# Performance work log

Hardware: AMD Instinct MI355X
Metric: run time of the kernel (lower is better)

Reference implementation:

```python
import jax, jax.numpy as jnp
import numpy as np

N_NODES = 50000
N_EDGES = 300000
HIDDEN = 256
Z_DIM = 128
N_LAYERS = 3
NUM_GRAPHS = 16
EPS = 1e-5


def setup_inputs() -> dict:
    key = jax.random.key(0)
    ks = jax.random.split(key, 16)
    s = 0.05
    inp = {
        "voxel_pos": jax.random.normal(ks[0], (N_NODES, 3), jnp.float32),
        "edge_index": jax.random.randint(ks[1], (2, N_EDGES), 0, N_NODES),
        "batch_index": jnp.sort(jax.random.randint(ks[2], (N_NODES,), 0, NUM_GRAPHS)),
        # input projection Linear(3, H) + GroupNorm(1, H) affine
        "W_in": jax.random.normal(ks[3], (3, HIDDEN), jnp.float32) * s,
        "b_in": jnp.zeros((HIDDEN,), jnp.float32),
        "g_in": jnp.ones((HIDDEN,), jnp.float32),
        "be_in": jnp.zeros((HIDDEN,), jnp.float32),
        # stacked GCNConv weights/biases and per-layer GroupNorm affines
        "conv_W": jax.random.normal(ks[4], (N_LAYERS, HIDDEN, HIDDEN), jnp.float32) * s,
        "conv_b": jnp.zeros((N_LAYERS, HIDDEN), jnp.float32),
        "gn_g": jnp.ones((N_LAYERS, HIDDEN), jnp.float32),
        "gn_b": jnp.zeros((N_LAYERS, HIDDEN), jnp.float32),
        # output MLP: Linear(H,H) -> ReLU -> GroupNorm -> Linear(H, Z)
        "W_o1": jax.random.normal(ks[5], (HIDDEN, HIDDEN), jnp.float32) * s,
        "b_o1": jnp.zeros((HIDDEN,), jnp.float32),
        "g_o": jnp.ones((HIDDEN,), jnp.float32),
        "be_o": jnp.zeros((HIDDEN,), jnp.float32),
        "W_o2": jax.random.normal(ks[6], (HIDDEN, Z_DIM), jnp.float32) * s,
        "b_o2": jnp.zeros((Z_DIM,), jnp.float32),
    }
    return inp


def group_norm(x, g, b):
    # GroupNorm(1, C) on (N, C): normalize over channels per node (biased var)
    mu = jnp.mean(x, axis=-1, keepdims=True)
    var = jnp.mean(jnp.square(x - mu), axis=-1, keepdims=True)
    return (x - mu) * jax.lax.rsqrt(var + EPS) * g + b


def reference(voxel_pos, edge_index, batch_index, W_in, b_in, g_in, be_in,
              conv_W, conv_b, gn_g, gn_b, W_o1, b_o1, g_o, be_o, W_o2, b_o2):
    n = voxel_pos.shape[0]
    loop = jnp.arange(n, dtype=edge_index.dtype)
    src = jnp.concatenate([edge_index[0], loop])  # A + I self-loops (PyG GCNConv default)
    dst = jnp.concatenate([edge_index[1], loop])
    deg = jax.ops.segment_sum(jnp.ones_like(dst, jnp.float32), dst, num_segments=n)
    dinv = jnp.where(deg > 0, jax.lax.rsqrt(jnp.maximum(deg, 1.0)), 0.0)
    enorm = dinv[src] * dinv[dst]  # D^{-1/2} (A+I) D^{-1/2} edge weights

    # input_proj: Linear -> ReLU -> GroupNorm
    x = group_norm(jax.nn.relu(voxel_pos @ W_in + b_in), g_in, be_in)

    for l in range(N_LAYERS):
        identity = x
        h = x @ conv_W[l]                      # GCNConv linear transform
        msg = h[src] * enorm[:, None]          # gather + scale (E+N, H)
        h = jax.ops.segment_sum(msg, dst, num_segments=n) + conv_b[l]
        x = jax.nn.relu(group_norm(h, gn_g[l], gn_b[l])) + identity

    # global mean pool per graph
    summed = jax.ops.segment_sum(x, batch_index, num_segments=NUM_GRAPHS)
    counts = jax.ops.segment_sum(jnp.ones((n,), jnp.float32), batch_index, num_segments=NUM_GRAPHS)
    pooled = summed / jnp.maximum(counts, 1.0)[:, None]

    h = group_norm(jax.nn.relu(pooled @ W_o1 + b_o1), g_o, be_o)
    return h @ W_o2 + b_o2
```

## Files before the change

### kernel.cpp

```cpp
#include <hip/hip_runtime.h>
#include <hip/hip_bf16.h>

#define N_NODES 50000
#define N_EDGES 300000
#define HIDDEN 256
#define ZDIM 128
#define NLAYERS 3
#define NGRAPHS 16
#define EPS 1e-5f
#define NSCANBLK 196

#define OFF_POS    0
#define OFF_WIN    150000
#define OFF_BIN    150768
#define OFF_GIN    151024
#define OFF_BEIN   151280
#define OFF_CONVB  348144
#define OFF_GNG    348912
#define OFF_GNB    349680
#define OFF_WO1    350448
#define OFF_BO1    415984
#define OFF_GO     416240
#define OFF_BEO    416496
#define OFF_WO2    416752
#define OFF_BO2    449520
#define PARAMS_TOTAL 449648

typedef __attribute__((ext_vector_type(8))) short short8;
typedef __attribute__((ext_vector_type(4))) float floatx4;

__device__ inline float wave_reduce_sum(float v){
#pragma unroll
  for (int off = 32; off; off >>= 1) v += __shfl_xor(v, off);
  return v;
}

__device__ inline ushort f2bf(float f){
  __hip_bfloat16 t = __float2bfloat16(f);
  return *(ushort*)&t;
}
__device__ inline float bflo(unsigned int u){ return __uint_as_float(u << 16); }
__device__ inline float bfhi(unsigned int u){ return __uint_as_float(u & 0xffff0000u); }

__device__ inline void gload_lds16(const void* g, void* l){
  __builtin_amdgcn_global_load_lds((const __attribute__((address_space(1))) void*)g,
                                   (__attribute__((address_space(3))) void*)l, 16, 0, 0);
}

struct PrepArgs { const void* src[14]; int n[14]; int off[14]; const void* win; const void* convw; };

__global__ __launch_bounds__(256) void k_prep(PrepArgs a, float* __restrict__ params,
                                              ushort* __restrict__ Wt, int* __restrict__ flag){
  __shared__ int sf;
  int tid = threadIdx.x;
  if (tid == 0) sf = 0;
  __syncthreads();
  const unsigned short* w = (const unsigned short*)a.win;
  for (int i = tid; i < 768; i += 256){
    int e = (w[i] >> 7) & 0xff;
    if (e >= 148) atomicOr(&sf, 1);
  }
  __syncthreads();
  const bool isf32 = (sf != 0);
  if (blockIdx.x == 0 && tid == 0) *flag = sf;

  int stride = gridDim.x * blockDim.x;
  int t0 = blockIdx.x * blockDim.x + tid;
  for (int s = 0; s < 14; ++s){
    const void* src = a.src[s];
    int n = a.n[s];
    float* dst = params + a.off[s];
    if (isf32){
      const float* f = (const float*)src;
      for (int i = t0; i < n; i += stride) dst[i] = f[i];
    } else {
      const unsigned short* u = (const unsigned short*)src;
      for (int i = t0; i < n; i += stride) dst[i] = bflo(u[i]);
    }
  }
  for (int idx = t0; idx < NLAYERS * 65536; idx += stride){
    int l = idx >> 16, rem = idx & 65535, n = rem >> 8, k = rem & 255;
    int si = l * 65536 + k * 256 + n;
    float v = isf32 ? ((const float*)a.convw)[si] : bflo(((const unsigned short*)a.convw)[si]);
    Wt[idx] = f2bf(v);
  }
}

__global__ void k_init(int* __restrict__ deg, int* __restrict__ fill,
                       float* __restrict__ pooled, float* __restrict__ counts){
  int i = blockIdx.x * blockDim.x + threadIdx.x;
  if (i < N_NODES){ deg[i] = 1; fill[i] = 0; }
  if (i < NGRAPHS * 256) pooled[i] = 0.f;
  if (i < NGRAPHS) counts[i] = 0.f;
}

__global__ void k_deg(const int* __restrict__ dst, int* __restrict__ deg){
  int e = blockIdx.x * blockDim.x + threadIdx.x;
  if (e < N_EDGES) atomicAdd(&deg[dst[e]], 1);
}

__global__ __launch_bounds__(256) void k_scan1(const int* __restrict__ deg, int* __restrict__ row_start,
                                               int* __restrict__ bsum, float* __restrict__ dinv){
  __shared__ int sd[256];
  int tid = threadIdx.x;
  int i = blockIdx.x * 256 + tid;
  int v = (i < N_NODES) ? deg[i] : 0;
  if (i < N_NODES) dinv[i] = rsqrtf((float)v);
  sd[tid] = v;
  __syncthreads();
#pragma unroll
  for (int off = 1; off < 256; off <<= 1){
    int t = (tid >= off) ? sd[tid - off] : 0;
    __syncthreads();
    sd[tid] += t;
    __syncthreads();
  }
  if (i < N_NODES) row_start[i] = sd[tid];
  if (tid == 255) bsum[blockIdx.x] = sd[255];
}

__global__ __launch_bounds__(256) void k_scan2(const int* __restrict__ bsum, int* __restrict__ boff,
                                               int* __restrict__ row_start){
  __shared__ int sd[256];
  int tid = threadIdx.x;
  int v = (tid < NSCANBLK) ? bsum[tid] : 0;
  sd[tid] = v;
  __syncthreads();
#pragma unroll
  for (int off = 1; off < 256; off <<= 1){
    int t = (tid >= off) ? sd[tid - off] : 0;
    __syncthreads();
    sd[tid] += t;
    __syncthreads();
  }
  if (tid < NSCANBLK) boff[tid] = sd[tid] - v;
  if (tid == NSCANBLK - 1) row_start[N_NODES] = sd[tid];
}

__global__ __launch_bounds__(256) void k_scan3(const int* __restrict__ deg, const int* __restrict__ boff,
                                               int* __restrict__ row_start){
  int i = blockIdx.x * 256 + threadIdx.x;
  if (i < N_NODES) row_start[i] = row_start[i] + boff[blockIdx.x] - deg[i];
}

__global__ void k_fill(const int* __restrict__ src, const int* __restrict__ dst,
                       const int* __restrict__ row_start, int* __restrict__ fill,
                       const float* __restrict__ dinv,
                       int* __restrict__ csr_src, float* __restrict__ csr_w){
  int t = blockIdx.x * blockDim.x + threadIdx.x;
  if (t >= N_EDGES + N_NODES) return;
  int s, d;
  if (t < N_EDGES){ s = src[t]; d = dst[t]; }
  else            { s = t - N_EDGES; d = s; }
  int pos = row_start[d] + atomicAdd(&fill[d], 1);
  csr_src[pos] = s;
  csr_w[pos] = dinv[s] * dinv[d];
}

__global__ __launch_bounds__(256) void k_input_proj(const float* __restrict__ params,
                                                    ushort* __restrict__ x_bf){
  int lane = threadIdx.x & 63;
  int node = (blockIdx.x << 2) + (threadIdx.x >> 6);
  if (node >= N_NODES) return;
  const float* pos = params + OFF_POS + node * 3;
  float px = pos[0], py = pos[1], pz = pos[2];
  int c = lane * 4;
  const float* w0 = params + OFF_WIN;
  float v[4];
#pragma unroll
  for (int j = 0; j < 4; ++j){
    float t = params[OFF_BIN + c + j];
    t = fmaf(px, w0[c + j], t);
    t = fmaf(py, w0[256 + c + j], t);
    t = fmaf(pz, w0[512 + c + j], t);
    v[j] = fmaxf(t, 0.f);
  }
  float s  = v[0] + v[1] + v[2] + v[3];
  float ss = v[0]*v[0] + v[1]*v[1] + v[2]*v[2] + v[3]*v[3];
  s = wave_reduce_sum(s); ss = wave_reduce_sum(ss);
  float mean = s * (1.f/256.f);
  float var  = ss * (1.f/256.f) - mean * mean;
  float inv  = rsqrtf(var + EPS);
  float4 o;
  o.x = (v[0]-mean)*inv*params[OFF_GIN+c+0] + params[OFF_BEIN+c+0];
  o.y = (v[1]-mean)*inv*params[OFF_GIN+c+1] + params[OFF_BEIN+c+1];
  o.z = (v[2]-mean)*inv*params[OFF_GIN+c+2] + params[OFF_BEIN+c+2];
  o.w = (v[3]-mean)*inv*params[OFF_GIN+c+3] + params[OFF_BEIN+c+3];
  ushort4 ob = { f2bf(o.x), f2bf(o.y), f2bf(o.z), f2bf(o.w) };
  *(ushort4*)(x_bf + node * 256 + c) = ob;
}

#define GBM 128
__global__ __launch_bounds__(256) void k_gemm_bf(const ushort* __restrict__ A, const ushort* __restrict__ Bt,
                                                 ushort* __restrict__ Cb, int M){
  __shared__ __align__(16) ushort Sh[2 * GBM * 64];
  ushort* As = Sh;
  ushort* Bs = Sh + GBM * 64;
  int tid = threadIdx.x;
  int wave = tid >> 6, lane = tid & 63;
  int wr = wave >> 1, wc = wave & 1;
  int row0 = blockIdx.y * GBM;
  int col0 = blockIdx.x * GBM;
  int q = lane >> 4, l15 = lane & 15;
  int srow = lane >> 3;
  int sg   = lane & 7;
  floatx4 acc[4][4] = {};
  for (int k0 = 0; k0 < 256; k0 += 64){
    __syncthreads();
#pragma unroll
    for (int t = 0; t < 4; ++t){
      int rg = wave * 4 + t;
      int r  = rg * 8 + srow;
      int gs = sg ^ (r & 7);
      const ushort* ga = A  + (size_t)(row0 + r) * 256 + k0 + gs * 8;
      const ushort* gb = Bt + (size_t)(col0 + r) * 256 + k0 + gs * 8;
      gload_lds16(ga, As + rg * 512);
      gload_lds16(gb, Bs + rg * 512);
    }
    __syncthreads();
#pragma unroll
    for (int kk = 0; kk < 64; kk += 32){
      short8 af[4], bfr[4];
#pragma unroll
      for (int i = 0; i < 4; ++i){
        int R = wr * 64 + i * 16 + l15;
        int bg = (kk >> 3) + q;
        af[i] = *(const short8*)(As + R * 64 + ((bg ^ (R & 7)) << 3));
      }
#pragma unroll
      for (int j = 0; j < 4; ++j){
        int C = wc * 64 + j * 16 + l15;
        int bg = (kk >> 3) + q;
        bfr[j] = *(const short8*)(Bs + C * 64 + ((bg ^ (C & 7)) << 3));
      }
#pragma unroll
      for (int i = 0; i < 4; ++i)
#pragma unroll
        for (int j = 0; j < 4; ++j)
          acc[i][j] = __builtin_amdgcn_mfma_f32_16x16x32_bf16(af[i], bfr[j], acc[i][j], 0, 0, 0);
    }
  }
#pragma unroll
  for (int i = 0; i < 4; ++i){
#pragma unroll
    for (int r = 0; r < 4; ++r){
      int row = row0 + wr * 64 + i * 16 + q * 4 + r;
      if (row < M){
#pragma unroll
        for (int j = 0; j < 4; ++j){
          int col = col0 + wc * 64 + j * 16 + l15;
          Cb[row * 256 + col] = f2bf(acc[i][j][r]);
        }
      }
    }
  }
}

__global__ __launch_bounds__(256) void k_agg_norm(const ushort* __restrict__ hb, ushort* __restrict__ x_bf,
    const int* __restrict__ row_start, const int* __restrict__ csr_src, const float* __restrict__ csr_w,
    const float* __restrict__ params, int layer){
  int lane = threadIdx.x & 63;
  int node = (blockIdx.x << 2) + (threadIdx.x >> 6);
  if (node >= N_NODES) return;
  int c = lane * 4;
  float a0 = 0.f, a1 = 0.f, a2 = 0.f, a3 = 0.f;
  int p0 = row_start[node], p1 = row_start[node + 1];
  int p = p0;
  for (; p + 4 <= p1; p += 4){
    int s0 = csr_src[p],     s1 = csr_src[p + 1];
    int s2 = csr_src[p + 2], s3 = csr_src[p + 3];
    float w0 = csr_w[p],     w1 = csr_w[p + 1];
    float w2 = csr_w[p + 2], w3 = csr_w[p + 3];
    uint2 v0 = *(const uint2*)(hb + (size_t)s0 * 256 + c);
    uint2 v1 = *(const uint2*)(hb + (size_t)s1 * 256 + c);
    uint2 v2 = *(const uint2*)(hb + (size_t)s2 * 256 + c);
    uint2 v3 = *(const uint2*)(hb + (size_t)s3 * 256 + c);
    a0 = fmaf(w0, bflo(v0.x), a0); a1 = fmaf(w0, bfhi(v0.x), a1);
    a2 = fmaf(w0, bflo(v0.y), a2); a3 = fmaf(w0, bfhi(v0.y), a3);
    a0 = fmaf(w1, bflo(v1.x), a0); a1 = fmaf(w1, bfhi(v1.x), a1);
    a2 = fmaf(w1, bflo(v1.y), a2); a3 = fmaf(w1, bfhi(v1.y), a3);
    a0 = fmaf(w2, bflo(v2.x), a0); a1 = fmaf(w2, bfhi(v2.x), a1);
    a2 = fmaf(w2, bflo(v2.y), a2); a3 = fmaf(w2, bfhi(v2.y), a3);
    a0 = fmaf(w3, bflo(v3.x), a0); a1 = fmaf(w3, bfhi(v3.x), a1);
    a2 = fmaf(w3, bflo(v3.y), a2); a3 = fmaf(w3, bfhi(v3.y), a3);
  }
  for (; p < p1; ++p){
    int s0 = csr_src[p];
    float w0 = csr_w[p];
    uint2 v0 = *(const uint2*)(hb + (size_t)s0 * 256 + c);
    a0 = fmaf(w0, bflo(v0.x), a0); a1 = fmaf(w0, bfhi(v0.x), a1);
    a2 = fmaf(w0, bflo(v0.y), a2); a3 = fmaf(w0, bfhi(v0.y), a3);
  }
  const float* cb = params + OFF_CONVB + layer * 256;
  float v[4] = { a0 + cb[c], a1 + cb[c+1], a2 + cb[c+2], a3 + cb[c+3] };
  float s  = v[0] + v[1] + v[2] + v[3];
  float ss = v[0]*v[0] + v[1]*v[1] + v[2]*v[2] + v[3]*v[3];
  s = wave_reduce_sum(s); ss = wave_reduce_sum(ss);
  float mean = s * (1.f/256.f);
  float var  = ss * (1.f/256.f) - mean * mean;
  float inv  = rsqrtf(var + EPS);
  const float* g = params + OFF_GNG + layer * 256;
  const float* b = params + OFF_GNB + layer * 256;
  uint2 xo = *(uint2*)(x_bf + (size_t)node * 256 + c);
  float o0 = fmaxf((v[0]-mean)*inv*g[c+0] + b[c+0], 0.f) + bflo(xo.x);
  float o1 = fmaxf((v[1]-mean)*inv*g[c+1] + b[c+1], 0.f) + bfhi(xo.x);
  float o2 = fmaxf((v[2]-mean)*inv*g[c+2] + b[c+2], 0.f) + bflo(xo.y);
  float o3 = fmaxf((v[3]-mean)*inv*g[c+3] + b[c+3], 0.f) + bfhi(xo.y);
  ushort4 ob = { f2bf(o0), f2bf(o1), f2bf(o2), f2bf(o3) };
  *(ushort4*)(x_bf + (size_t)node * 256 + c) = ob;
}

#define PBLK 256
__global__ __launch_bounds__(256) void k_pool(const ushort* __restrict__ x_bf, const int* __restrict__ batch,
                                              float* __restrict__ pooled, float* __restrict__ counts){
  __shared__ float lacc[NGRAPHS][256];
  __shared__ float lcnt[NGRAPHS];
  int tid = threadIdx.x;
  int wave = tid >> 6, lane = tid & 63;
  int c = lane * 4;
#pragma unroll
  for (int g = 0; g < NGRAPHS; ++g) lacc[g][tid] = 0.f;
  if (tid < NGRAPHS) lcnt[tid] = 0.f;
  __syncthreads();

  int n0 = blockIdx.x * PBLK + wave * 64;
  if (n0 < N_NODES){
    int n1 = min(n0 + 64, N_NODES);
    int b0 = batch[n0], b1 = batch[n1 - 1];
    float a0 = 0.f, a1 = 0.f, a2 = 0.f, a3 = 0.f;
    if (b0 == b1){
      int i = n0;
      for (; i + 8 <= n1; i += 8){
        uint2 v[8];
#pragma unroll
        for (int j = 0; j < 8; ++j) v[j] = *(const uint2*)(x_bf + (size_t)(i + j) * 256 + c);
#pragma unroll
        for (int j = 0; j < 8; ++j){
          a0 += bflo(v[j].x); a1 += bfhi(v[j].x);
          a2 += bflo(v[j].y); a3 += bfhi(v[j].y);
        }
      }
      for (; i < n1; ++i){
        uint2 v = *(const uint2*)(x_bf + (size_t)i * 256 + c);
        a0 += bflo(v.x); a1 += bfhi(v.x); a2 += bflo(v.y); a3 += bfhi(v.y);
      }
      atomicAdd(&lacc[b0][c + 0], a0); atomicAdd(&lacc[b0][c + 1], a1);
      atomicAdd(&lacc[b0][c + 2], a2); atomicAdd(&lacc[b0][c + 3], a3);
      if (lane == 0) atomicAdd(&lcnt[b0], (float)(n1 - n0));
    } else {
      int cur = b0, cnt = 0;
      for (int i = n0; i < n1; ++i){
        int g = batch[i];
        if (g != cur){
          atomicAdd(&lacc[cur][c + 0], a0); atomicAdd(&lacc[cur][c + 1], a1);
          atomicAdd(&lacc[cur][c + 2], a2); atomicAdd(&lacc[cur][c + 3], a3);
          if (lane == 0) atomicAdd(&lcnt[cur], (float)cnt);
          a0 = a1 = a2 = a3 = 0.f; cnt = 0; cur = g;
        }
        uint2 v = *(const uint2*)(x_bf + (size_t)i * 256 + c);
        a0 += bflo(v.x); a1 += bfhi(v.x); a2 += bflo(v.y); a3 += bfhi(v.y);
        cnt++;
      }
      atomicAdd(&lacc[cur][c + 0], a0); atomicAdd(&lacc[cur][c + 1], a1);
      atomicAdd(&lacc[cur][c + 2], a2); atomicAdd(&lacc[cur][c + 3], a3);
      if (lane == 0) atomicAdd(&lcnt[cur], (float)cnt);
    }
  }
  __syncthreads();

  int base = blockIdx.x * PBLK;
  if (base < N_NODES){
    int gmin = batch[base];
    int gmax = batch[min(base + PBLK, N_NODES) - 1];
    for (int g = gmin; g <= gmax; ++g){
      float v = lacc[g][tid];
      if (v != 0.f) atomicAdd(&pooled[g * 256 + tid], v);
      if (tid == 0 && lcnt[g] > 0.f) atomicAdd(&counts[g], lcnt[g]);
    }
  }
}

__global__ __launch_bounds__(256) void k_head(const float* __restrict__ pooled, const float* __restrict__ counts,
    const float* __restrict__ params, void* __restrict__ out, const int* __restrict__ flag){
  __shared__ float m[256];
  __shared__ float hh[256];
  __shared__ float red[2][4];
  int g = blockIdx.x, tid = threadIdx.x;
  float cnt = fmaxf(counts[g], 1.f);
  m[tid] = pooled[g * 256 + tid] / cnt;
  __syncthreads();
  const float* W1 = params + OFF_WO1;
  float acc = params[OFF_BO1 + tid];
  for (int k = 0; k < 256; ++k) acc = fmaf(m[k], W1[k * 256 + tid], acc);
  acc = fmaxf(acc, 0.f);
  float s = wave_reduce_sum(acc), ss = wave_reduce_sum(acc * acc);
  int wv = tid >> 6, lane = tid & 63;
  if (lane == 0){ red[0][wv] = s; red[1][wv] = ss; }
  __syncthreads();
  float S  = red[0][0] + red[0][1] + red[0][2] + red[0][3];
  float SS = red[1][0] + red[1][1] + red[1][2] + red[1][3];
  float mean = S * (1.f/256.f);
  float var  = SS * (1.f/256.f) - mean * mean;
  float inv  = rsqrtf(var + EPS);
  float hn = (acc - mean) * inv * params[OFF_GO + tid] + params[OFF_BEO + tid];
  hh[tid] = hn;
  __syncthreads();
  if (tid < ZDIM){
    const float* W2 = params + OFF_WO2;
    float o = params[OFF_BO2 + tid];
    for (int k = 0; k < 256; ++k) o = fmaf(hh[k], W2[k * 128 + tid], o);
    if (*flag) ((float*)out)[g * 128 + tid] = o;
    else       ((__hip_bfloat16*)out)[g * 128 + tid] = __float2bfloat16(o);
  }
}

extern "C" void kernel_launch(void* const* d_in, const int* in_sizes, int n_in,
                              void* d_out, int out_size, void* d_ws, size_t ws_size,
                              hipStream_t stream){
  size_t o = 0;
  auto alloc = [&](size_t bytes)->size_t{ size_t r = o; o = (o + bytes + 255) & ~(size_t)255; return r; };
  size_t off_flag   = alloc(4);
  size_t off_deg    = alloc((size_t)N_NODES * 4);
  size_t off_dinv   = alloc((size_t)N_NODES * 4);
  size_t off_rs     = alloc((size_t)(N_NODES + 1) * 4);
  size_t off_fill   = alloc((size_t)N_NODES * 4);
  size_t off_bsum   = alloc((size_t)NSCANBLK * 4);
  size_t off_boff   = alloc((size_t)NSCANBLK * 4);
  size_t off_csrs   = alloc((size_t)(N_EDGES + N_NODES) * 4);
  size_t off_csrw   = alloc((size_t)(N_EDGES + N_NODES) * 4);
  size_t off_params = alloc((size_t)PARAMS_TOTAL * 4);
  size_t off_xbf    = alloc((size_t)N_NODES * HIDDEN * 2);
  size_t off_hbf    = alloc((size_t)N_NODES * HIDDEN * 2);
  size_t off_wt     = alloc((size_t)NLAYERS * HIDDEN * HIDDEN * 2);
  size_t off_pool   = alloc((size_t)NGRAPHS * 256 * 4);
  size_t off_cnt    = alloc((size_t)NGRAPHS * 4);
  if (o > ws_size) return;

  char* ws = (char*)d_ws;
  int*    flag     = (int*)(ws + off_flag);
  int*    deg      = (int*)(ws + off_deg);
  float*  dinv     = (float*)(ws + off_dinv);
  int*    row_start= (int*)(ws + off_rs);
  int*    fill     = (int*)(ws + off_fill);
  int*    bsum     = (int*)(ws + off_bsum);
  int*    boff     = (int*)(ws + off_boff);
  int*    csr_src  = (int*)(ws + off_csrs);
  float*  csr_w    = (float*)(ws + off_csrw);
  float*  params   = (float*)(ws + off_params);
  ushort* x_bf     = (ushort*)(ws + off_xbf);
  ushort* h_bf     = (ushort*)(ws + off_hbf);
  ushort* Wt       = (ushort*)(ws + off_wt);
  float*  pooled   = (float*)(ws + off_pool);
  float*  counts   = (float*)(ws + off_cnt);

  const int* edge_src = (const int*)d_in[1];
  const int* edge_dst = (const int*)d_in[1] + N_EDGES;
  const int* batch    = (const int*)d_in[2];

  PrepArgs pa;
  const int srcIdx[14] = {0,3,4,5,6,8,9,10,11,12,13,14,15,16};
  const int ns[14]     = {150000,768,256,256,256,768,768,768,65536,256,256,256,32768,128};
  const int offs[14]   = {OFF_POS,OFF_WIN,OFF_BIN,OFF_GIN,OFF_BEIN,OFF_CONVB,OFF_GNG,OFF_GNB,
                          OFF_WO1,OFF_BO1,OFF_GO,OFF_BEO,OFF_WO2,OFF_BO2};
  for (int i = 0; i < 14; ++i){ pa.src[i] = d_in[srcIdx[i]]; pa.n[i] = ns[i]; pa.off[i] = offs[i]; }
  pa.win = d_in[3]; pa.convw = d_in[7];
  k_prep<<<512, 256, 0, stream>>>(pa, params, Wt, flag);

  k_init<<<(N_NODES + 255) / 256, 256, 0, stream>>>(deg, fill, pooled, counts);
  k_deg<<<(N_EDGES + 255) / 256, 256, 0, stream>>>(edge_dst, deg);
  k_scan1<<<NSCANBLK, 256, 0, stream>>>(deg, row_start, bsum, dinv);
  k_scan2<<<1, 256, 0, stream>>>(bsum, boff, row_start);
  k_scan3<<<NSCANBLK, 256, 0, stream>>>(deg, boff, row_start);
  k_fill<<<(N_EDGES + N_NODES + 255) / 256, 256, 0, stream>>>(edge_src, edge_dst, row_start, fill,
                                                              dinv, csr_src, csr_w);
  k_input_proj<<<N_NODES / 4, 256, 0, stream>>>(params, x_bf);

  dim3 ggrid(2, (N_NODES + GBM - 1) / GBM);
  for (int l = 0; l < NLAYERS; ++l){
    k_gemm_bf<<<ggrid, 256, 0, stream>>>(x_bf, Wt + l * 65536, h_bf, N_NODES);
    k_agg_norm<<<N_NODES / 4, 256, 0, stream>>>(h_bf, x_bf, row_start, csr_src, csr_w, params, l);
  }

  k_pool<<<(N_NODES + PBLK - 1) / PBLK, 256, 0, stream>>>(x_bf, batch, pooled, counts);
  k_head<<<NGRAPHS, 256, 0, stream>>>(pooled, counts, params, d_out, flag);
}
```

Before: 352.7 us.

## Fuse aggregation, GEMM and GroupNorm into one per-layer kernel via aggregate-first reorder

Each GCN layer now aggregates neighbour features first (A·X), stores the aggregated rows for a 64-node tile in shared memory, multiplies by the layer weight with MFMA, then applies bias, GroupNorm, ReLU and the residual in the epilogue, with ping-pong x buffers. This removes the intermediate h round trip through global memory and one kernel launch per layer. The trade-offs are that the aggregated features are rounded to bf16 before the GEMM, the whole weight matrix is streamed per 64-row block, epilogue stores are scalar 2-byte writes, and the large shared-memory footprint may lower occupancy for the latency-bound gather.

```diff
diff --git a/kernel.cpp b/kernel.cpp
--- a/kernel.cpp
+++ b/kernel.cpp
@@ -190,46 +190,86 @@
   *(ushort4*)(x_bf + node * 256 + c) = ob;
 }
 
-#define GBM 128
-__global__ __launch_bounds__(256) void k_gemm_bf(const ushort* __restrict__ A, const ushort* __restrict__ Bt,
-                                                 ushort* __restrict__ Cb, int M){
-  __shared__ __align__(16) ushort Sh[2 * GBM * 64];
-  ushort* As = Sh;
-  ushort* Bs = Sh + GBM * 64;
+#define LBM 64
+__global__ __launch_bounds__(256) void k_layer(const ushort* __restrict__ xin, ushort* __restrict__ xout,
+    const int* __restrict__ row_start, const int* __restrict__ csr_src, const float* __restrict__ csr_w,
+    const ushort* __restrict__ Bt, const float* __restrict__ params, int layer){
+  __shared__ __align__(16) ushort As[LBM * 256];
+  __shared__ __align__(16) ushort Bs[256 * 64];
+  __shared__ float rsum[4][LBM], rsq[4][LBM];
+  __shared__ float mmean[LBM], minv[LBM];
   int tid = threadIdx.x;
   int wave = tid >> 6, lane = tid & 63;
-  int wr = wave >> 1, wc = wave & 1;
-  int row0 = blockIdx.y * GBM;
-  int col0 = blockIdx.x * GBM;
   int q = lane >> 4, l15 = lane & 15;
-  int srow = lane >> 3;
-  int sg   = lane & 7;
+  int srow = lane >> 3, sg = lane & 7;
+  int row0 = blockIdx.x * LBM;
+
+#pragma unroll
+  for (int t = 0; t < 8; ++t){
+    int rg = wave * 8 + t;
+    int r = rg * 8 + srow;
+    int gs = sg ^ (r & 7);
+    gload_lds16(Bt + (size_t)r * 256 + 0 + gs * 8, Bs + rg * 512);
+  }
+
+  int c = lane * 4;
+  for (int t = 0; t < 16; ++t){
+    int nloc = wave * 16 + t;
+    int node = row0 + nloc;
+    float a0 = 0.f, a1 = 0.f, a2 = 0.f, a3 = 0.f;
+    if (node < N_NODES){
+      int p0 = row_start[node], p1 = row_start[node + 1];
+      int p = p0;
+      for (; p + 8 <= p1; p += 8){
+        int s[8]; float w[8]; uint2 v[8];
+#pragma unroll
+        for (int j = 0; j < 8; ++j){ s[j] = csr_src[p + j]; w[j] = csr_w[p + j]; }
+#pragma unroll
+        for (int j = 0; j < 8; ++j) v[j] = *(const uint2*)(xin + (size_t)s[j] * 256 + c);
+#pragma unroll
+        for (int j = 0; j < 8; ++j){
+          a0 = fmaf(w[j], bflo(v[j].x), a0); a1 = fmaf(w[j], bfhi(v[j].x), a1);
+          a2 = fmaf(w[j], bflo(v[j].y), a2); a3 = fmaf(w[j], bfhi(v[j].y), a3);
+        }
+      }
+      for (; p < p1; ++p){
+        int s0 = csr_src[p]; float w0 = csr_w[p];
+        uint2 v0 = *(const uint2*)(xin + (size_t)s0 * 256 + c);
+        a0 = fmaf(w0, bflo(v0.x), a0); a1 = fmaf(w0, bfhi(v0.x), a1);
+        a2 = fmaf(w0, bflo(v0.y), a2); a3 = fmaf(w0, bfhi(v0.y), a3);
+      }
+    }
+    int gp = (lane >> 1) ^ (nloc & 7);
+    ushort4 mv = { f2bf(a0), f2bf(a1), f2bf(a2), f2bf(a3) };
+    *(ushort4*)(As + nloc * 256 + gp * 8 + (lane & 1) * 4) = mv;
+  }
+  __syncthreads();
+
   floatx4 acc[4][4] = {};
   for (int k0 = 0; k0 < 256; k0 += 64){
-    __syncthreads();
-#pragma unroll
-    for (int t = 0; t < 4; ++t){
-      int rg = wave * 4 + t;
-      int r  = rg * 8 + srow;
-      int gs = sg ^ (r & 7);
-      const ushort* ga = A  + (size_t)(row0 + r) * 256 + k0 + gs * 8;
-      const ushort* gb = Bt + (size_t)(col0 + r) * 256 + k0 + gs * 8;
-      gload_lds16(ga, As + rg * 512);
-      gload_lds16(gb, Bs + rg * 512);
-    }
-    __syncthreads();
+    if (k0 > 0){
+      __syncthreads();
+#pragma unroll
+      for (int t = 0; t < 8; ++t){
+        int rg = wave * 8 + t;
+        int r = rg * 8 + srow;
+        int gs = sg ^ (r & 7);
+        gload_lds16(Bt + (size_t)r * 256 + k0 + gs * 8, Bs + rg * 512);
+      }
+      __syncthreads();
+    }
 #pragma unroll
     for (int kk = 0; kk < 64; kk += 32){
       short8 af[4], bfr[4];
 #pragma unroll
       for (int i = 0; i < 4; ++i){
-        int R = wr * 64 + i * 16 + l15;
-        int bg = (kk >> 3) + q;
-        af[i] = *(const short8*)(As + R * 64 + ((bg ^ (R & 7)) << 3));
+        int R = i * 16 + l15;
+        int lg = ((k0 + kk) >> 3) + q;
+        af[i] = *(const short8*)(As + R * 256 + ((lg ^ (R & 7)) << 3));
       }
 #pragma unroll
       for (int j = 0; j < 4; ++j){
-        int C = wc * 64 + j * 16 + l15;
+        int C = wave * 64 + j * 16 + l15;
         int bg = (kk >> 3) + q;
         bfr[j] = *(const short8*)(Bs + C * 64 + ((bg ^ (C & 7)) << 3));
       }
@@ -240,74 +280,78 @@
           acc[i][j] = __builtin_amdgcn_mfma_f32_16x16x32_bf16(af[i], bfr[j], acc[i][j], 0, 0, 0);
     }
   }
+
+  const float* cb = params + OFF_CONVB + layer * 256;
+  const float* gw = params + OFF_GNG  + layer * 256;
+  const float* bw = params + OFF_GNB  + layer * 256;
+  float cbv[4], gv[4], bv[4];
+#pragma unroll
+  for (int j = 0; j < 4; ++j){
+    int C = wave * 64 + j * 16 + l15;
+    cbv[j] = cb[C]; gv[j] = gw[C]; bv[j] = bw[C];
+  }
+  float psum[4][4], psq[4][4];
+#pragma unroll
+  for (int i = 0; i < 4; ++i)
+#pragma unroll
+    for (int r = 0; r < 4; ++r){
+      float s = 0.f, s2 = 0.f;
+#pragma unroll
+      for (int j = 0; j < 4; ++j){
+        float v = acc[i][j][r] + cbv[j];
+        acc[i][j][r] = v;
+        s += v; s2 += v * v;
+      }
+      psum[i][r] = s; psq[i][r] = s2;
+    }
+#pragma unroll
+  for (int off = 1; off < 16; off <<= 1){
+#pragma unroll
+    for (int i = 0; i < 4; ++i)
+#pragma unroll
+      for (int r = 0; r < 4; ++r){
+        psum[i][r] += __shfl_xor(psum[i][r], off);
+        psq[i][r]  += __shfl_xor(psq[i][r], off);
+      }
+  }
+  if (l15 == 0){
+#pragma unroll
+    for (int i = 0; i < 4; ++i)
+#pragma unroll
+      for (int r = 0; r < 4; ++r){
+        int row = i * 16 + q * 4 + r;
+        rsum[wave][row] = psum[i][r];
+        rsq[wave][row]  = psq[i][r];
+      }
+  }
+  __syncthreads();
+  if (tid < LBM){
+    float t0 = rsum[0][tid] + rsum[1][tid] + rsum[2][tid] + rsum[3][tid];
+    float t1 = rsq[0][tid]  + rsq[1][tid]  + rsq[2][tid]  + rsq[3][tid];
+    float mean = t0 * (1.f/256.f);
+    float var  = t1 * (1.f/256.f) - mean * mean;
+    mmean[tid] = mean;
+    minv[tid]  = rsqrtf(var + EPS);
+  }
+  __syncthreads();
 #pragma unroll
   for (int i = 0; i < 4; ++i){
 #pragma unroll
     for (int r = 0; r < 4; ++r){
-      int row = row0 + wr * 64 + i * 16 + q * 4 + r;
-      if (row < M){
+      int row = i * 16 + q * 4 + r;
+      int grow = row0 + row;
+      if (grow < N_NODES){
+        float mean = mmean[row], inv = minv[row];
 #pragma unroll
         for (int j = 0; j < 4; ++j){
-          int col = col0 + wc * 64 + j * 16 + l15;
-          Cb[row * 256 + col] = f2bf(acc[i][j][r]);
+          int col = wave * 64 + j * 16 + l15;
+          float vn = (acc[i][j][r] - mean) * inv * gv[j] + bv[j];
+          float o = fmaxf(vn, 0.f) + bflo((unsigned int)xin[(size_t)grow * 256 + col]);
+          xout[(size_t)grow * 256 + col] = f2bf(o);
         }
       }
     }
   }
-}
-
-__global__ __launch_bounds__(256) void k_agg_norm(const ushort* __restrict__ hb, ushort* __restrict__ x_bf,
-    const int* __restrict__ row_start, const int* __restrict__ csr_src, const float* __restrict__ csr_w,
-    const float* __restrict__ params, int layer){
-  int lane = threadIdx.x & 63;
-  int node = (blockIdx.x << 2) + (threadIdx.x >> 6);
-  if (node >= N_NODES) return;
-  int c = lane * 4;
-  float a0 = 0.f, a1 = 0.f, a2 = 0.f, a3 = 0.f;
-  int p0 = row_start[node], p1 = row_start[node + 1];
-  int p = p0;
-  for (; p + 4 <= p1; p += 4){
-    int s0 = csr_src[p],     s1 = csr_src[p + 1];
-    int s2 = csr_src[p + 2], s3 = csr_src[p + 3];
-    float w0 = csr_w[p],     w1 = csr_w[p + 1];
-    float w2 = csr_w[p + 2], w3 = csr_w[p + 3];
-    uint2 v0 = *(const uint2*)(hb + (size_t)s0 * 256 + c);
-    uint2 v1 = *(const uint2*)(hb + (size_t)s1 * 256 + c);
-    uint2 v2 = *(const uint2*)(hb + (size_t)s2 * 256 + c);
-    uint2 v3 = *(const uint2*)(hb + (size_t)s3 * 256 + c);
-    a0 = fmaf(w0, bflo(v0.x), a0); a1 = fmaf(w0, bfhi(v0.x), a1);
-    a2 = fmaf(w0, bflo(v0.y), a2); a3 = fmaf(w0, bfhi(v0.y), a3);
-    a0 = fmaf(w1, bflo(v1.x), a0); a1 = fmaf(w1, bfhi(v1.x), a1);
-    a2 = fmaf(w1, bflo(v1.y), a2); a3 = fmaf(w1, bfhi(v1.y), a3);
-    a0 = fmaf(w2, bflo(v2.x), a0); a1 = fmaf(w2, bfhi(v2.x), a1);
-    a2 = fmaf(w2, bflo(v2.y), a2); a3 = fmaf(w2, bfhi(v2.y), a3);
-    a0 = fmaf(w3, bflo(v3.x), a0); a1 = fmaf(w3, bfhi(v3.x), a1);
-    a2 = fmaf(w3, bflo(v3.y), a2); a3 = fmaf(w3, bfhi(v3.y), a3);
-  }
-  for (; p < p1; ++p){
-    int s0 = csr_src[p];
-    float w0 = csr_w[p];
-    uint2 v0 = *(const uint2*)(hb + (size_t)s0 * 256 + c);
-    a0 = fmaf(w0, bflo(v0.x), a0); a1 = fmaf(w0, bfhi(v0.x), a1);
-    a2 = fmaf(w0, bflo(v0.y), a2); a3 = fmaf(w0, bfhi(v0.y), a3);
-  }
-  const float* cb = params + OFF_CONVB + layer * 256;
-  float v[4] = { a0 + cb[c], a1 + cb[c+1], a2 + cb[c+2], a3 + cb[c+3] };
-  float s  = v[0] + v[1] + v[2] + v[3];
-  float ss = v[0]*v[0] + v[1]*v[1] + v[2]*v[2] + v[3]*v[3];
-  s = wave_reduce_sum(s); ss = wave_reduce_sum(ss);
-  float mean = s * (1.f/256.f);
-  float var  = ss * (1.f/256.f) - mean * mean;
-  float inv  = rsqrtf(var + EPS);
-  const float* g = params + OFF_GNG + layer * 256;
-  const float* b = params + OFF_GNB + layer * 256;
-  uint2 xo = *(uint2*)(x_bf + (size_t)node * 256 + c);
-  float o0 = fmaxf((v[0]-mean)*inv*g[c+0] + b[c+0], 0.f) + bflo(xo.x);
-  float o1 = fmaxf((v[1]-mean)*inv*g[c+1] + b[c+1], 0.f) + bfhi(xo.x);
-  float o2 = fmaxf((v[2]-mean)*inv*g[c+2] + b[c+2], 0.f) + bflo(xo.y);
-  float o3 = fmaxf((v[3]-mean)*inv*g[c+3] + b[c+3], 0.f) + bfhi(xo.y);
-  ushort4 ob = { f2bf(o0), f2bf(o1), f2bf(o2), f2bf(o3) };
-  *(ushort4*)(x_bf + (size_t)node * 256 + c) = ob;
 }
 
 #define PBLK 256
@@ -429,8 +473,8 @@
   size_t off_csrs   = alloc((size_t)(N_EDGES + N_NODES) * 4);
   size_t off_csrw   = alloc((size_t)(N_EDGES + N_NODES) * 4);
   size_t off_params = alloc((size_t)PARAMS_TOTAL * 4);
-  size_t off_xbf    = alloc((size_t)N_NODES * HIDDEN * 2);
-  size_t off_hbf    = alloc((size_t)N_NODES * HIDDEN * 2);
+  size_t off_x0     = alloc((size_t)N_NODES * HIDDEN * 2);
+  size_t off_x1     = alloc((size_t)N_NODES * HIDDEN * 2);
   size_t off_wt     = alloc((size_t)NLAYERS * HIDDEN * HIDDEN * 2);
   size_t off_pool   = alloc((size_t)NGRAPHS * 256 * 4);
   size_t off_cnt    = alloc((size_t)NGRAPHS * 4);
@@ -447,8 +491,8 @@
   int*    csr_src  = (int*)(ws + off_csrs);
   float*  csr_w    = (float*)(ws + off_csrw);
   float*  params   = (float*)(ws + off_params);
-  ushort* x_bf     = (ushort*)(ws + off_xbf);
-  ushort* h_bf     = (ushort*)(ws + off_hbf);
+  ushort* x0       = (ushort*)(ws + off_x0);
+  ushort* x1       = (ushort*)(ws + off_x1);
   ushort* Wt       = (ushort*)(ws + off_wt);
   float*  pooled   = (float*)(ws + off_pool);
   float*  counts   = (float*)(ws + off_cnt);
@@ -473,14 +517,13 @@
   k_scan3<<<NSCANBLK, 256, 0, stream>>>(deg, boff, row_start);
   k_fill<<<(N_EDGES + N_NODES + 255) / 256, 256, 0, stream>>>(edge_src, edge_dst, row_start, fill,
                                                               dinv, csr_src, csr_w);
-  k_input_proj<<<N_NODES / 4, 256, 0, stream>>>(params, x_bf);
-
-  dim3 ggrid(2, (N_NODES + GBM - 1) / GBM);
-  for (int l = 0; l < NLAYERS; ++l){
-    k_gemm_bf<<<ggrid, 256, 0, stream>>>(x_bf, Wt + l * 65536, h_bf, N_NODES);
-    k_agg_norm<<<N_NODES / 4, 256, 0, stream>>>(h_bf, x_bf, row_start, csr_src, csr_w, params, l);
-  }
-
-  k_pool<<<(N_NODES + PBLK - 1) / PBLK, 256, 0, stream>>>(x_bf, batch, pooled, counts);
+  k_input_proj<<<N_NODES / 4, 256, 0, stream>>>(params, x0);
+
+  int nlb = (N_NODES + LBM - 1) / LBM;
+  k_layer<<<nlb, 256, 0, stream>>>(x0, x1, row_start, csr_src, csr_w, Wt + 0 * 65536, params, 0);
+  k_layer<<<nlb, 256, 0, stream>>>(x1, x0, row_start, csr_src, csr_w, Wt + 1 * 65536, params, 1);
+  k_layer<<<nlb, 256, 0, stream>>>(x0, x1, row_start, csr_src, csr_w, Wt + 2 * 65536, params, 2);
+
+  k_pool<<<(N_NODES + PBLK - 1) / PBLK, 256, 0, stream>>>(x1, batch, pooled, counts);
   k_head<<<NGRAPHS, 256, 0, stream>>>(pooled, counts, params, d_out, flag);
 }
```

Result: slower. 553.6 us (+57.0%).
